# Performance work log

Hardware: AMD Instinct MI355X
Metric: run time of the kernel (lower is better)

The kernel has to match this reference:

```python
import jax, jax.numpy as jnp
import numpy as np

N = 50000
E = 800000
F_IN = 256
C = 64  # embedding_size, heads=1
EDGE_DIM = 2
NEG_SLOPE = 0.01


def setup_inputs() -> dict:
    key = jax.random.key(0)
    ks = jax.random.split(key, 12)
    s = 1.0 / np.sqrt(C)
    return {
        "x": jax.random.normal(ks[0], (N, F_IN), jnp.float32),
        "edge_index": jax.random.randint(ks[1], (2, E), 0, N, jnp.int64),
        "edge_attr": jax.random.normal(ks[2], (E, EDGE_DIM), jnp.float32),
        "Wf": jax.random.normal(ks[3], (F_IN, C), jnp.float32) / np.sqrt(F_IN),
        "bf": jnp.zeros((C,), jnp.float32),
        "Wq": jax.random.normal(ks[4], (C, C), jnp.float32) * s,
        "bq": jnp.zeros((C,), jnp.float32),
        "Wk": jax.random.normal(ks[5], (C, C), jnp.float32) * s,
        "bk": jnp.zeros((C,), jnp.float32),
        "Wv": jax.random.normal(ks[6], (C, C), jnp.float32) * s,
        "bv": jnp.zeros((C,), jnp.float32),
        "We": jax.random.normal(ks[7], (EDGE_DIM, C), jnp.float32) / np.sqrt(EDGE_DIM),
        "Wskip": jax.random.normal(ks[8], (C, C), jnp.float32) * s,
        "bskip": jnp.zeros((C,), jnp.float32),
    }


def reference(x, edge_index, edge_attr, Wf, bf, Wq, bq, Wk, bk, Wv, bv, We, Wskip, bskip):
    n = x.shape[0]
    src, dst = edge_index[0], edge_index[1]
    inv_sqrt_c = 1.0 / np.sqrt(C)

    h = jax.nn.leaky_relu(x @ Wf + bf, NEG_SLOPE)
    e = edge_attr @ We  # [E, C] edge embedding (lin_edge, no bias), same each layer

    for _ in range(3):
        q = h @ Wq + bq
        k = h @ Wk + bk
        v = h @ Wv + bv
        kj = k[src] + e                                  # [E, C] key + edge feat
        alpha = jnp.sum(q[dst] * kj, axis=-1) * inv_sqrt_c  # [E]
        # per-destination softmax
        m = jax.ops.segment_max(alpha, dst, num_segments=n)
        ex = jnp.exp(alpha - m[dst])
        den = jax.ops.segment_sum(ex, dst, num_segments=n)
        a = ex / den[dst]                                # [E]
        msg = (v[src] + e) * a[:, None]                  # [E, C]
        agg = jax.ops.segment_sum(msg, dst, num_segments=n)  # [N, C]
        h = jax.nn.leaky_relu(agg + h @ Wskip + bskip, NEG_SLOPE)  # root_weight skip
    return h
```

## Files before the change

kernel.cpp:

```cpp
#include <hip/hip_runtime.h>
#include <hip/hip_fp16.h>

#define NN 50000
#define NE 800000
#define FIN 256
#define C 64
#define NEG_SLOPE 0.01f
#define SCAN_BLOCKS ((NN + 255) / 256)
#define NBUCK 196
#define BCAP 8192
#define EB_CHUNK 2048
#define EB_BLOCKS ((NE + EB_CHUNK - 1) / EB_CHUNK)

typedef float f32x16 __attribute__((ext_vector_type(16)));

__device__ __forceinline__ float leaky(float v) { return v > 0.f ? v : NEG_SLOPE * v; }

__global__ __launch_bounds__(256) void k_tw(const float* __restrict__ Wq,
                                            const float* __restrict__ Wk,
                                            const float* __restrict__ Wv,
                                            const float* __restrict__ Ws,
                                            float* __restrict__ Wt) {
    const int idx = blockIdx.x * 256 + threadIdx.x;
    if (idx >= 4 * 64 * 64) return;
    const int m = idx >> 12, r = idx & 4095, c = r >> 6, k = r & 63;
    const float* W = (m == 0) ? Wq : (m == 1) ? Wk : (m == 2) ? Wv : Ws;
    Wt[idx] = W[k * 64 + c];
}

__global__ __launch_bounds__(256) void k_feat(const float* __restrict__ x,
                                              const float* __restrict__ Wf,
                                              const float* __restrict__ bf,
                                              float* __restrict__ h) {
    __shared__ float4 Sx[64][33];
    const int t = threadIdx.x;
    const int lane = t & 63;
    const int q = __builtin_amdgcn_readfirstlane(t) >> 6;
    const int base = blockIdx.x * 64;

    const float4* x4 = (const float4*)x;
    float4 acc[4];
#pragma unroll
    for (int cp = 0; cp < 4; ++cp) acc[cp] = make_float4(0.f, 0.f, 0.f, 0.f);

#define FRAG(wreg, xs)                                                      \
    acc[0].x = fmaf(xs, wreg[0],  acc[0].x);                                \
    acc[0].y = fmaf(xs, wreg[1],  acc[0].y);                                \
    acc[0].z = fmaf(xs, wreg[2],  acc[0].z);                                \
    acc[0].w = fmaf(xs, wreg[3],  acc[0].w);                                \
    acc[1].x = fmaf(xs, wreg[4],  acc[1].x);                                \
    acc[1].y = fmaf(xs, wreg[5],  acc[1].y);                                \
    acc[1].z = fmaf(xs, wreg[6],  acc[1].z);                                \
    acc[1].w = fmaf(xs, wreg[7],  acc[1].w);                                \
    acc[2].x = fmaf(xs, wreg[8],  acc[2].x);                                \
    acc[2].y = fmaf(xs, wreg[9],  acc[2].y);                                \
    acc[2].z = fmaf(xs, wreg[10], acc[2].z);                                \
    acc[2].w = fmaf(xs, wreg[11], acc[2].w);                                \
    acc[3].x = fmaf(xs, wreg[12], acc[3].x);                                \
    acc[3].y = fmaf(xs, wreg[13], acc[3].y);                                \
    acc[3].z = fmaf(xs, wreg[14], acc[3].z);                                \
    acc[3].w = fmaf(xs, wreg[15], acc[3].w);

    for (int ph = 0; ph < 2; ++ph) {
#pragma unroll
        for (int i = 0; i < 8; ++i) {
            const int idx = t + i * 256;
            const int row = idx >> 5, c = idx & 31;
            int nn = base + row; if (nn >= NN) nn = NN - 1;
            Sx[row][c] = x4[(size_t)nn * 64 + ph * 32 + c];
        }
        __syncthreads();

        const float* wbase = Wf + (size_t)(ph * 128) * 64 + q * 16;
#pragma unroll
        for (int j = 0; j < 32; ++j) {
            const float4 xv = Sx[lane][j];
            const float* wrow = wbase + (size_t)j * 256;
            f32x16 w0_, w1_, w2_, w3_;
            asm volatile("s_load_dwordx16 %0, %4, 0x0\n\t"
                         "s_load_dwordx16 %1, %4, 0x100\n\t"
                         "s_load_dwordx16 %2, %4, 0x200\n\t"
                         "s_load_dwordx16 %3, %4, 0x300\n\t"
                         "s_waitcnt lgkmcnt(0)"
                         : "=&s"(w0_), "=&s"(w1_), "=&s"(w2_), "=&s"(w3_)
                         : "s"(wrow));
            FRAG(w0_, xv.x)
            FRAG(w1_, xv.y)
            FRAG(w2_, xv.z)
            FRAG(w3_, xv.w)
        }
        __syncthreads();
    }
#undef FRAG

    float4* O = (float4*)Sx;
    const float4* bf4 = (const float4*)bf;
#pragma unroll
    for (int cp = 0; cp < 4; ++cp) {
        const float4 b = bf4[q * 4 + cp];
        float4 r;
        r.x = leaky(acc[cp].x + b.x); r.y = leaky(acc[cp].y + b.y);
        r.z = leaky(acc[cp].z + b.z); r.w = leaky(acc[cp].w + b.w);
        O[lane * 17 + q * 4 + cp] = r;
    }
    __syncthreads();
#pragma unroll
    for (int i = 0; i < 4; ++i) {
        const int idx = t + i * 256;
        const int row = idx >> 4, c = idx & 15;
        const int nn = base + row;
        if (nn < NN) ((float4*)h)[(size_t)nn * 16 + c] = O[row * 17 + c];
    }
}

#define QKVS_NPB 32

__global__ __launch_bounds__(256) void k_qkvs(const float* __restrict__ h,
                                              const float* __restrict__ Wt,
                                              const float* __restrict__ bq,
                                              const float* __restrict__ bk,
                                              const float* __restrict__ bv,
                                              const float* __restrict__ bs,
                                              float* __restrict__ qkvs) {
    const int t = threadIdx.x;
    const int lane = t & 63;
    const int sec = __builtin_amdgcn_readfirstlane(t) >> 6;
    const int base = blockIdx.x * QKVS_NPB;

    int m, cidx;
    float bias;
    if (sec == 0)      { m = 0; cidx = lane; bias = bq[lane]; }
    else if (sec == 1) { m = 3; cidx = lane; bias = bs[lane]; }
    else {
        cidx = ((sec - 2) << 5) + (lane >> 1);
        m = 1 + (lane & 1);
        bias = (lane & 1) ? bv[cidx] : bk[cidx];
    }

    const float4* wb = (const float4*)(Wt + ((size_t)m << 12) + ((size_t)cidx << 6));
    float4 w[16];
#pragma unroll
    for (int j = 0; j < 16; ++j) w[j] = wb[j];

    const int nmax = (base + QKVS_NPB <= NN) ? QKVS_NPB : (NN - base);
    for (int i = 0; i < nmax; ++i) {
        const float* hrow = h + (size_t)(base + i) * 64;
        f32x16 ha, hb, hc, hd;
        asm volatile("s_load_dwordx16 %0, %4, 0x0\n\t"
                     "s_load_dwordx16 %1, %4, 0x40\n\t"
                     "s_load_dwordx16 %2, %4, 0x80\n\t"
                     "s_load_dwordx16 %3, %4, 0xc0\n\t"
                     "s_waitcnt lgkmcnt(0)"
                     : "=&s"(ha), "=&s"(hb), "=&s"(hc), "=&s"(hd)
                     : "s"(hrow));
        float a0 = 0.f, a1 = 0.f, a2 = 0.f, a3 = 0.f;
#pragma unroll
        for (int j = 0; j < 4; ++j) {
            a0 = fmaf(ha[4 * j + 0], w[j].x, a0);
            a1 = fmaf(ha[4 * j + 1], w[j].y, a1);
            a2 = fmaf(ha[4 * j + 2], w[j].z, a2);
            a3 = fmaf(ha[4 * j + 3], w[j].w, a3);
        }
#pragma unroll
        for (int j = 0; j < 4; ++j) {
            a0 = fmaf(hb[4 * j + 0], w[4 + j].x, a0);
            a1 = fmaf(hb[4 * j + 1], w[4 + j].y, a1);
            a2 = fmaf(hb[4 * j + 2], w[4 + j].z, a2);
            a3 = fmaf(hb[4 * j + 3], w[4 + j].w, a3);
        }
#pragma unroll
        for (int j = 0; j < 4; ++j) {
            a0 = fmaf(hc[4 * j + 0], w[8 + j].x, a0);
            a1 = fmaf(hc[4 * j + 1], w[8 + j].y, a1);
            a2 = fmaf(hc[4 * j + 2], w[8 + j].z, a2);
            a3 = fmaf(hc[4 * j + 3], w[8 + j].w, a3);
        }
#pragma unroll
        for (int j = 0; j < 4; ++j) {
            a0 = fmaf(hd[4 * j + 0], w[12 + j].x, a0);
            a1 = fmaf(hd[4 * j + 1], w[12 + j].y, a1);
            a2 = fmaf(hd[4 * j + 2], w[12 + j].z, a2);
            a3 = fmaf(hd[4 * j + 3], w[12 + j].w, a3);
        }
        const float val = ((a0 + a1) + (a2 + a3)) + bias;
        float* orow = qkvs + (size_t)(base + i) * 192;
        if (sec == 0) {
            orow[lane] = val;
        } else if (sec == 1) {
            orow[128 + lane] = val;
        } else {
            __half* kvh = (__half*)(orow + 64);
            kvh[((sec - 2) << 6) + lane] = __float2half(val);
        }
    }
}

__global__ __launch_bounds__(256) void k_bucket(const int* __restrict__ ei,
                                                const float* __restrict__ eattr,
                                                int* __restrict__ gcur,
                                                uint2* __restrict__ ebuck) {
    __shared__ int hist[NBUCK], lbase[NBUCK], lcur[NBUCK];
    const int t = threadIdx.x;
    const int base = blockIdx.x * EB_CHUNK;
    if (t < NBUCK) { hist[t] = 0; lcur[t] = 0; }
    __syncthreads();

    int dcache[8];
#pragma unroll
    for (int i = 0; i < 8; ++i) {
        const int e = base + i * 256 + t;
        int d = -1;
        if (e < NE) {
            d = ei[NE + e];
            atomicAdd(&hist[d >> 8], 1);
        }
        dcache[i] = d;
    }
    __syncthreads();
    if (t < NBUCK && hist[t] > 0)
        lbase[t] = atomicAdd(&gcur[t], hist[t]);
    __syncthreads();

#pragma unroll
    for (int i = 0; i < 8; ++i) {
        const int e = base + i * 256 + t;
        const int d = dcache[i];
        if (d >= 0) {
            const int b = d >> 8;
            const int rank = atomicAdd(&lcur[b], 1);
            const __half2 a = __floats2half2_rn(eattr[e * 2], eattr[e * 2 + 1]);
            const unsigned src = (unsigned)ei[e];
            ebuck[(size_t)b * BCAP + lbase[b] + rank] =
                make_uint2(((unsigned)d << 16) | src, *(const unsigned*)&a);
        }
    }
}

__global__ __launch_bounds__(256) void k_fin_deg(const int* __restrict__ gcur,
                                                 const uint2* __restrict__ ebuck,
                                                 int* __restrict__ deg) {
    __shared__ int dcnt[256];
    const int t = threadIdx.x;
    const int b = blockIdx.x;
    dcnt[t] = 0;
    __syncthreads();
    const int n = gcur[b];
    for (int i = t; i < n; i += 256) {
        const unsigned x = ebuck[(size_t)b * BCAP + i].x;
        atomicAdd(&dcnt[(x >> 16) & 255], 1);
    }
    __syncthreads();
    const int idx = b * 256 + t;
    if (idx < NN) deg[idx] = dcnt[t];
}

__global__ __launch_bounds__(256) void k_blocksum(const int* __restrict__ deg,
                                                  int* __restrict__ bsum) {
    __shared__ int sh[256];
    const int t = threadIdx.x;
    const int idx = blockIdx.x * 256 + t;
    sh[t] = (idx < NN) ? deg[idx] : 0;
    __syncthreads();
#pragma unroll
    for (int off = 128; off > 0; off >>= 1) {
        if (t < off) sh[t] += sh[t + off];
        __syncthreads();
    }
    if (t == 0) bsum[blockIdx.x] = sh[0];
}

__global__ __launch_bounds__(256) void k_scanb(const int* __restrict__ bsum,
                                               int* __restrict__ boff) {
    __shared__ int sh[256];
    const int t = threadIdx.x;
    const int v = (t < SCAN_BLOCKS) ? bsum[t] : 0;
    sh[t] = v;
    __syncthreads();
#pragma unroll
    for (int off = 1; off < 256; off <<= 1) {
        const int x = (t >= off) ? sh[t - off] : 0;
        __syncthreads();
        sh[t] += x;
        __syncthreads();
    }
    if (t < SCAN_BLOCKS) boff[t] = sh[t] - v;
}

__global__ __launch_bounds__(256) void k_writeptr(const int* __restrict__ deg,
                                                  const int* __restrict__ boff,
                                                  int* __restrict__ row_ptr) {
    __shared__ int sh[256];
    const int t = threadIdx.x;
    const int idx = blockIdx.x * 256 + t;
    const int v = (idx < NN) ? deg[idx] : 0;
    sh[t] = v;
    __syncthreads();
#pragma unroll
    for (int off = 1; off < 256; off <<= 1) {
        const int x = (t >= off) ? sh[t - off] : 0;
        __syncthreads();
        sh[t] += x;
        __syncthreads();
    }
    if (idx < NN) row_ptr[idx] = boff[blockIdx.x] + sh[t] - v;
    if (idx == 0) row_ptr[NN] = NE;
}

__global__ __launch_bounds__(256) void k_fin_scat(const int* __restrict__ gcur,
                                                  const uint2* __restrict__ ebuck,
                                                  const int* __restrict__ row_ptr,
                                                  uint2* __restrict__ erec) {
    __shared__ int pcur[256];
    const int t = threadIdx.x;
    const int b = blockIdx.x;
    const int idx = b * 256 + t;
    pcur[t] = (idx < NN) ? row_ptr[idx] : 0;
    __syncthreads();
    const int n = gcur[b];
    for (int i = t; i < n; i += 256) {
        const uint2 rec = ebuck[(size_t)b * BCAP + i];
        const int d = (rec.x >> 16) & 255;
        const int pos = atomicAdd(&pcur[d], 1);
        erec[pos] = make_uint2(rec.x & 0xFFFFu, rec.y);
    }
}

__global__ __launch_bounds__(256) void k_conv(const int* __restrict__ row_ptr,
                                              const uint2* __restrict__ erec,
                                              const float* __restrict__ We,
                                              const float* __restrict__ qkvs,
                                              float* __restrict__ hout) {
    const int t = threadIdx.x;
    const int lane = t & 63;
    const int g = lane >> 4;
    const int p = lane & 15;
    const int wv = __builtin_amdgcn_readfirstlane(t) >> 6;
    const int d = blockIdx.x * 4 + wv;
    if (d >= NN) return;

    const float* qrow = qkvs + (size_t)d * 192;
    const float4 q4  = *(const float4*)(qrow + 4 * p);
    const float4 w0  = *(const float4*)(We + 4 * p);
    const float4 w1  = *(const float4*)(We + 64 + 4 * p);

    float pg0 = q4.x * w0.x + q4.y * w0.y + q4.z * w0.z + q4.w * w0.w;
    float pg1 = q4.x * w1.x + q4.y * w1.y + q4.z * w1.z + q4.w * w1.w;
#pragma unroll
    for (int mask = 1; mask <= 8; mask <<= 1) {
        pg0 += __shfl_xor(pg0, mask);
        pg1 += __shfl_xor(pg1, mask);
    }
    const float g0 = pg0, g1 = pg1;

    const int i0 = row_ptr[d], i1 = row_ptr[d + 1];
    const char* kvbase = (const char*)qkvs + 256 + ((size_t)p << 4);

    float m = -1e30f, l = 0.f, S1 = 0.f, S2 = 0.f;
    float4 acc = make_float4(0.f, 0.f, 0.f, 0.f);

    int i = i0 + g;
    for (; i + 4 < i1; i += 8) {
        const uint2 ra = erec[i];
        const uint2 rb = erec[i + 4];
        const __half2 aha = *(const __half2*)&ra.y;
        const __half2 ahb = *(const __half2*)&rb.y;
        const float a0a = __low2float(aha), a1a = __high2float(aha);
        const float a0b = __low2float(ahb), a1b = __high2float(ahb);
        const float4 kva = *(const float4*)(kvbase + (size_t)ra.x * 768);
        const float4 kvb = *(const float4*)(kvbase + (size_t)rb.x * 768);
        const __half2* ha = (const __half2*)&kva;
        const __half2* hb = (const __half2*)&kvb;
        const float ka0 = __low2float(ha[0]), va0 = __high2float(ha[0]);
        const float ka1 = __low2float(ha[1]), va1 = __high2float(ha[1]);
        const float ka2 = __low2float(ha[2]), va2 = __high2float(ha[2]);
        const float ka3 = __low2float(ha[3]), va3 = __high2float(ha[3]);
        const float kb0 = __low2float(hb[0]), vb0 = __high2float(hb[0]);
        const float kb1 = __low2float(hb[1]), vb1 = __high2float(hb[1]);
        const float kb2 = __low2float(hb[2]), vb2 = __high2float(hb[2]);
        const float kb3 = __low2float(hb[3]), vb3 = __high2float(hb[3]);
        float da = q4.x * ka0 + q4.y * ka1 + q4.z * ka2 + q4.w * ka3;
        float db = q4.x * kb0 + q4.y * kb1 + q4.z * kb2 + q4.w * kb3;
        da += __shfl_xor(da, 1);  db += __shfl_xor(db, 1);
        da += __shfl_xor(da, 2);  db += __shfl_xor(db, 2);
        da += __shfl_xor(da, 4);  db += __shfl_xor(db, 4);
        da += __shfl_xor(da, 8);  db += __shfl_xor(db, 8);
        const float Pa = (da + g0 * a0a + g1 * a1a) * 0.125f;
        const float Pb = (db + g0 * a0b + g1 * a1b) * 0.125f;
        const float mn = fmaxf(m, fmaxf(Pa, Pb));
        const float s  = __expf(m - mn);
        const float ea = __expf(Pa - mn);
        const float eb = __expf(Pb - mn);
        l = l * s + ea + eb;
        acc.x = acc.x * s + va0 * ea + vb0 * eb;
        acc.y = acc.y * s + va1 * ea + vb1 * eb;
        acc.z = acc.z * s + va2 * ea + vb2 * eb;
        acc.w = acc.w * s + va3 * ea + vb3 * eb;
        S1 = S1 * s + a0a * ea + a0b * eb;
        S2 = S2 * s + a1a * ea + a1b * eb;
        m = mn;
    }
    for (; i < i1; i += 4) {
        const uint2 r = erec[i];
        const __half2 ah = *(const __half2*)&r.y;
        const float a0 = __low2float(ah), a1 = __high2float(ah);
        const float4 kvl = *(const float4*)(kvbase + (size_t)r.x * 768);
        const __half2* hv = (const __half2*)&kvl;
        const float kf0 = __low2float(hv[0]), vf0 = __high2float(hv[0]);
        const float kf1 = __low2float(hv[1]), vf1 = __high2float(hv[1]);
        const float kf2 = __low2float(hv[2]), vf2 = __high2float(hv[2]);
        const float kf3 = __low2float(hv[3]), vf3 = __high2float(hv[3]);
        float dot = q4.x * kf0 + q4.y * kf1 + q4.z * kf2 + q4.w * kf3;
        dot += __shfl_xor(dot, 1);
        dot += __shfl_xor(dot, 2);
        dot += __shfl_xor(dot, 4);
        dot += __shfl_xor(dot, 8);
        const float P = (dot + g0 * a0 + g1 * a1) * 0.125f;
        const float mn = fmaxf(m, P);
        const float s = __expf(m - mn);
        const float e = __expf(P - mn);
        l = l * s + e;
        acc.x = acc.x * s + vf0 * e;
        acc.y = acc.y * s + vf1 * e;
        acc.z = acc.z * s + vf2 * e;
        acc.w = acc.w * s + vf3 * e;
        S1 = S1 * s + a0 * e;
        S2 = S2 * s + a1 * e;
        m = mn;
    }

#pragma unroll
    for (int mask = 16; mask <= 32; mask <<= 1) {
        const float mo  = __shfl_xor(m, mask);
        const float lo  = __shfl_xor(l, mask);
        const float axo = __shfl_xor(acc.x, mask);
        const float ayo = __shfl_xor(acc.y, mask);
        const float azo = __shfl_xor(acc.z, mask);
        const float awo = __shfl_xor(acc.w, mask);
        const float S1o = __shfl_xor(S1, mask);
        const float S2o = __shfl_xor(S2, mask);
        const float mn = fmaxf(m, mo);
        const float sA = __expf(m - mn);
        const float sB = __expf(mo - mn);
        l     = l * sA + lo * sB;
        acc.x = acc.x * sA + axo * sB;
        acc.y = acc.y * sA + ayo * sB;
        acc.z = acc.z * sA + azo * sB;
        acc.w = acc.w * sA + awo * sB;
        S1    = S1 * sA + S1o * sB;
        S2    = S2 * sA + S2o * sB;
        m = mn;
    }

    if (lane < 16) {
        const float inv = (l > 0.f) ? 1.f / l : 0.f;
        const float4 sk = *(const float4*)(qrow + 128 + 4 * p);
        float4 r;
        r.x = leaky((acc.x + S1 * w0.x + S2 * w1.x) * inv + sk.x);
        r.y = leaky((acc.y + S1 * w0.y + S2 * w1.y) * inv + sk.y);
        r.z = leaky((acc.z + S1 * w0.z + S2 * w1.z) * inv + sk.z);
        r.w = leaky((acc.w + S1 * w0.w + S2 * w1.w) * inv + sk.w);
        *(float4*)(hout + (size_t)d * C + 4 * p) = r;
    }
}

extern "C" void kernel_launch(void* const* d_in, const int* in_sizes, int n_in,
                              void* d_out, int out_size, void* d_ws, size_t ws_size,
                              hipStream_t stream) {
    const float* x     = (const float*)d_in[0];
    const int*   ei    = (const int*)d_in[1];
    const float* eattr = (const float*)d_in[2];
    const float* Wf    = (const float*)d_in[3];
    const float* bf    = (const float*)d_in[4];
    const float* Wq    = (const float*)d_in[5];
    const float* bq    = (const float*)d_in[6];
    const float* Wk    = (const float*)d_in[7];
    const float* bk    = (const float*)d_in[8];
    const float* Wv    = (const float*)d_in[9];
    const float* bv    = (const float*)d_in[10];
    const float* We    = (const float*)d_in[11];
    const float* Ws    = (const float*)d_in[12];
    const float* bs    = (const float*)d_in[13];
    float* out = (float*)d_out;

    char* p = (char*)d_ws;
    float*  h       = (float*)p;  p += (size_t)NN * C * 4;
    float*  qkvs    = (float*)p;  p += (size_t)NN * 192 * 4;
    float*  Wt      = (float*)p;  p += (size_t)4 * 64 * 64 * 4;
    int*    deg     = (int*)p;    p += (size_t)NN * 4;
    int*    row_ptr = (int*)p;    p += (size_t)(NN + 1) * 4;
    int*    bsum    = (int*)p;    p += (size_t)SCAN_BLOCKS * 4;
    int*    boff    = (int*)p;    p += (size_t)SCAN_BLOCKS * 4;
    int*    gcur    = (int*)p;    p += (size_t)NBUCK * 4;
    uint2*  erec    = (uint2*)p;  p += (size_t)NE * 8;
    uint2*  ebuck   = (uint2*)p;  p += (size_t)NBUCK * BCAP * 8;

    k_tw<<<64, 256, 0, stream>>>(Wq, Wk, Wv, Ws, Wt);
    hipMemsetAsync(gcur, 0, (size_t)NBUCK * 4, stream);
    k_bucket<<<EB_BLOCKS, 256, 0, stream>>>(ei, eattr, gcur, ebuck);
    k_fin_deg<<<NBUCK, 256, 0, stream>>>(gcur, ebuck, deg);
    k_blocksum<<<SCAN_BLOCKS, 256, 0, stream>>>(deg, bsum);
    k_scanb<<<1, 256, 0, stream>>>(bsum, boff);
    k_writeptr<<<SCAN_BLOCKS, 256, 0, stream>>>(deg, boff, row_ptr);
    k_fin_scat<<<NBUCK, 256, 0, stream>>>(gcur, ebuck, row_ptr, erec);

    const int feat_grid = (NN + 63) / 64;
    const int qkvs_grid = (NN + QKVS_NPB - 1) / QKVS_NPB;

    k_feat<<<feat_grid, 256, 0, stream>>>(x, Wf, bf, h);

    for (int layer = 0; layer < 3; ++layer) {
        k_qkvs<<<qkvs_grid, 256, 0, stream>>>(h, Wt, bq, bk, bv, bs, qkvs);
        float* hout = (layer == 2) ? out : h;
        k_conv<<<(NN + 3) / 4, 256, 0, stream>>>(row_ptr, erec, We, qkvs, hout);
    }
}
```

Baseline: 426.4 us.

## Stage node rows in LDS and compute two projections per wave in QKVS kernel

The QKVS projection kernel now loads the block's 32 node rows into shared memory once, replacing per-row scalar s_load sequences that each waited on lgkmcnt. Work is re-split so each wave handles 16 nodes and two output matrices (K and V, or Q and skip), holding two weight columns in registers. Each LDS read of h therefore feeds two dot products, and K/V are written as packed half2. The cost is roughly double the weight registers per thread, which may lower occupancy, plus a block-wide barrier.

```diff
diff --git a/kernel.cpp b/kernel.cpp
--- a/kernel.cpp
+++ b/kernel.cpp
@@ -122,75 +122,59 @@
                                               const float* __restrict__ bv,
                                               const float* __restrict__ bs,
                                               float* __restrict__ qkvs) {
+    __shared__ float4 Sh[QKVS_NPB][16];
     const int t = threadIdx.x;
     const int lane = t & 63;
-    const int sec = __builtin_amdgcn_readfirstlane(t) >> 6;
+    const int wid = __builtin_amdgcn_readfirstlane(t) >> 6;
     const int base = blockIdx.x * QKVS_NPB;
 
-    int m, cidx;
-    float bias;
-    if (sec == 0)      { m = 0; cidx = lane; bias = bq[lane]; }
-    else if (sec == 1) { m = 3; cidx = lane; bias = bs[lane]; }
-    else {
-        cidx = ((sec - 2) << 5) + (lane >> 1);
-        m = 1 + (lane & 1);
-        bias = (lane & 1) ? bv[cidx] : bk[cidx];
-    }
-
-    const float4* wb = (const float4*)(Wt + ((size_t)m << 12) + ((size_t)cidx << 6));
-    float4 w[16];
-#pragma unroll
-    for (int j = 0; j < 16; ++j) w[j] = wb[j];
-
-    const int nmax = (base + QKVS_NPB <= NN) ? QKVS_NPB : (NN - base);
-    for (int i = 0; i < nmax; ++i) {
-        const float* hrow = h + (size_t)(base + i) * 64;
-        f32x16 ha, hb, hc, hd;
-        asm volatile("s_load_dwordx16 %0, %4, 0x0\n\t"
-                     "s_load_dwordx16 %1, %4, 0x40\n\t"
-                     "s_load_dwordx16 %2, %4, 0x80\n\t"
-                     "s_load_dwordx16 %3, %4, 0xc0\n\t"
-                     "s_waitcnt lgkmcnt(0)"
-                     : "=&s"(ha), "=&s"(hb), "=&s"(hc), "=&s"(hd)
-                     : "s"(hrow));
+    const float4* h4 = (const float4*)h;
+#pragma unroll
+    for (int i = 0; i < 2; ++i) {
+        const int idx = t + i * 256;
+        const int row = idx >> 4, c = idx & 15;
+        int n = base + row; if (n >= NN) n = NN - 1;
+        Sh[row][c] = h4[(size_t)n * 16 + c];
+    }
+
+    const bool kv = (wid < 2);
+    const int wn = (wid & 1) << 4;
+
+    const int mA = kv ? 1 : 0;
+    const int mB = kv ? 2 : 3;
+    const float4* wa4 = (const float4*)(Wt + ((size_t)mA << 12) + ((size_t)lane << 6));
+    const float4* wb4 = (const float4*)(Wt + ((size_t)mB << 12) + ((size_t)lane << 6));
+    float4 wa[16], wb[16];
+#pragma unroll
+    for (int j = 0; j < 16; ++j) { wa[j] = wa4[j]; wb[j] = wb4[j]; }
+    const float biasA = kv ? bk[lane] : bq[lane];
+    const float biasB = kv ? bv[lane] : bs[lane];
+
+    __syncthreads();
+
+#pragma unroll 2
+    for (int i = 0; i < 16; ++i) {
+        const int n = base + wn + i;
         float a0 = 0.f, a1 = 0.f, a2 = 0.f, a3 = 0.f;
-#pragma unroll
-        for (int j = 0; j < 4; ++j) {
-            a0 = fmaf(ha[4 * j + 0], w[j].x, a0);
-            a1 = fmaf(ha[4 * j + 1], w[j].y, a1);
-            a2 = fmaf(ha[4 * j + 2], w[j].z, a2);
-            a3 = fmaf(ha[4 * j + 3], w[j].w, a3);
+        float b0 = 0.f, b1 = 0.f, b2 = 0.f, b3 = 0.f;
+#pragma unroll
+        for (int j = 0; j < 16; ++j) {
+            const float4 xv = Sh[wn + i][j];
+            a0 = fmaf(xv.x, wa[j].x, a0); a1 = fmaf(xv.y, wa[j].y, a1);
+            a2 = fmaf(xv.z, wa[j].z, a2); a3 = fmaf(xv.w, wa[j].w, a3);
+            b0 = fmaf(xv.x, wb[j].x, b0); b1 = fmaf(xv.y, wb[j].y, b1);
+            b2 = fmaf(xv.z, wb[j].z, b2); b3 = fmaf(xv.w, wb[j].w, b3);
         }
-#pragma unroll
-        for (int j = 0; j < 4; ++j) {
-            a0 = fmaf(hb[4 * j + 0], w[4 + j].x, a0);
-            a1 = fmaf(hb[4 * j + 1], w[4 + j].y, a1);
-            a2 = fmaf(hb[4 * j + 2], w[4 + j].z, a2);
-            a3 = fmaf(hb[4 * j + 3], w[4 + j].w, a3);
-        }
-#pragma unroll
-        for (int j = 0; j < 4; ++j) {
-            a0 = fmaf(hc[4 * j + 0], w[8 + j].x, a0);
-            a1 = fmaf(hc[4 * j + 1], w[8 + j].y, a1);
-            a2 = fmaf(hc[4 * j + 2], w[8 + j].z, a2);
-            a3 = fmaf(hc[4 * j + 3], w[8 + j].w, a3);
-        }
-#pragma unroll
-        for (int j = 0; j < 4; ++j) {
-            a0 = fmaf(hd[4 * j + 0], w[12 + j].x, a0);
-            a1 = fmaf(hd[4 * j + 1], w[12 + j].y, a1);
-            a2 = fmaf(hd[4 * j + 2], w[12 + j].z, a2);
-            a3 = fmaf(hd[4 * j + 3], w[12 + j].w, a3);
-        }
-        const float val = ((a0 + a1) + (a2 + a3)) + bias;
-        float* orow = qkvs + (size_t)(base + i) * 192;
-        if (sec == 0) {
-            orow[lane] = val;
-        } else if (sec == 1) {
-            orow[128 + lane] = val;
-        } else {
-            __half* kvh = (__half*)(orow + 64);
-            kvh[((sec - 2) << 6) + lane] = __float2half(val);
+        const float A = ((a0 + a1) + (a2 + a3)) + biasA;
+        const float B = ((b0 + b1) + (b2 + b3)) + biasB;
+        if (n < NN) {
+            float* orow = qkvs + (size_t)n * 192;
+            if (kv) {
+                ((__half2*)(orow + 64))[lane] = __floats2half2_rn(A, B);
+            } else {
+                orow[lane] = A;
+                orow[128 + lane] = B;
+            }
         }
     }
 }
```

Result: slower. 463.1 us (+8.6%).
